# Performance work log

Hardware: AMD Instinct MI355X
Metric: run time of the kernel (lower is better)

## Reference

```python
import jax, jax.numpy as jnp
import numpy as np

IMG_FEAT = 2048
HIDDEN = 1024
K_TIMES = 3
GLIMPSE = 8
BA_HIDDEN = K_TIMES * HIDDEN  # 3072


def setup_inputs() -> dict:
    key = jax.random.key(0)
    ks = jax.random.split(key, 9)
    b, n_v, n_q = 64, 128, 32
    v = jax.random.normal(ks[0], (b, n_v, IMG_FEAT), dtype=jnp.float32)
    q = jax.random.normal(ks[1], (b, n_q, HIDDEN), dtype=jnp.float32)
    # weight-normed Linear params (weight_norm with dim=None -> scalar g)
    v_w = jax.random.normal(ks[2], (BA_HIDDEN, IMG_FEAT), dtype=jnp.float32) * 0.02
    v_g = jnp.asarray(jnp.linalg.norm(v_w), dtype=jnp.float32)
    v_b = jnp.zeros((BA_HIDDEN,), dtype=jnp.float32)
    q_w = jax.random.normal(ks[3], (BA_HIDDEN, HIDDEN), dtype=jnp.float32) * 0.02
    q_g = jnp.asarray(jnp.linalg.norm(q_w), dtype=jnp.float32)
    q_b = jnp.zeros((BA_HIDDEN,), dtype=jnp.float32)
    h_mat = jax.random.normal(ks[4], (1, GLIMPSE, 1, BA_HIDDEN), dtype=jnp.float32)
    h_bias = jax.random.normal(ks[5], (1, GLIMPSE, 1, 1), dtype=jnp.float32)
    return {"v": v, "q": q, "v_w": v_w, "v_g": v_g, "v_b": v_b,
            "q_w": q_w, "q_g": q_g, "q_b": q_b,
            "h_mat": h_mat, "h_bias": h_bias}


def _wn_linear_relu(x, w, g, b):
    # weight_norm(dim=None): w_eff = g * w / ||w||_F (scalar g)
    w_eff = (g / jnp.linalg.norm(w)) * w
    return jax.nn.relu(jnp.einsum('bnd,kd->bnk', x, w_eff) + b)


def reference(v, q, v_w, v_g, v_b, q_w, q_g, q_b, h_mat, h_bias):
    # dropout layers are identity in eval mode
    v_ = _wn_linear_relu(v, v_w, v_g, v_b)  # [b, n_v, K]
    q_ = _wn_linear_relu(q, q_w, q_g, q_b)  # [b, n_q, K]
    # einsum('xhyk,bvk,bqk->bhvq') with h_mat [1,g,1,K]
    hm = h_mat[0, :, 0, :]  # [g, K]
    logits = jnp.einsum('hk,bvk,bqk->bhvq', hm, v_, q_) + h_bias
    return logits
```

## Files before the change

kernel.cpp:

```cpp
#include <hip/hip_runtime.h>

typedef __attribute__((ext_vector_type(8))) __bf16 bf16x8;
typedef __attribute__((ext_vector_type(4))) float f32x4;
typedef const __attribute__((address_space(1))) unsigned int gas_u32;
typedef __attribute__((address_space(3))) unsigned int las_u32;

__device__ __forceinline__ unsigned short f2bf(float f) {
  unsigned u = __builtin_bit_cast(unsigned, f);
  u = (u + 0x7FFFu + ((u >> 16) & 1u)) >> 16;
  return (unsigned short)u;
}
__device__ __forceinline__ float bf2f(unsigned short h) {
  return __builtin_bit_cast(float, (unsigned)h << 16);
}

__global__ __launch_bounds__(256) void k_prep(
    const float* __restrict__ v, const float* __restrict__ q,
    const float* __restrict__ vw, const float* __restrict__ qw,
    unsigned short* __restrict__ v_bf, unsigned short* __restrict__ q_bf,
    unsigned short* __restrict__ vw_bf, unsigned short* __restrict__ qw_bf,
    float* __restrict__ ss) {
  __shared__ float red[4];
  int bid = blockIdx.x, tid = threadIdx.x;
  const float* in;
  unsigned short* out;
  float* ssout = nullptr;
  int n8, b0, nb;
  if (bid < 896) {
    in = v; out = v_bf; n8 = 2097152; b0 = bid; nb = 896;
  } else if (bid < 1008) {
    in = q; out = q_bf; n8 = 262144; b0 = bid - 896; nb = 112;
  } else if (bid < 1360) {
    in = vw; out = vw_bf; n8 = 786432; b0 = bid - 1008; nb = 352; ssout = ss + 0;
  } else {
    in = qw; out = qw_bf; n8 = 393216; b0 = bid - 1360; nb = 176; ssout = ss + 1;
  }
  float s = 0.f;
  for (int i = b0 * 256 + tid; i < n8; i += nb * 256) {
    float4 a = ((const float4*)in)[2 * i];
    float4 b = ((const float4*)in)[2 * i + 1];
    if (ssout) {
      s += a.x * a.x + a.y * a.y + a.z * a.z + a.w * a.w;
      s += b.x * b.x + b.y * b.y + b.z * b.z + b.w * b.w;
    }
    uint4 o;
    o.x = f2bf(a.x) | ((unsigned)f2bf(a.y) << 16);
    o.y = f2bf(a.z) | ((unsigned)f2bf(a.w) << 16);
    o.z = f2bf(b.x) | ((unsigned)f2bf(b.y) << 16);
    o.w = f2bf(b.z) | ((unsigned)f2bf(b.w) << 16);
    ((uint4*)out)[i] = o;
  }
  if (ssout) {
    for (int off = 32; off; off >>= 1) s += __shfl_down(s, off);
    if ((tid & 63) == 0) red[tid >> 6] = s;
    __syncthreads();
    if (tid == 0) atomicAdd(ssout, red[0] + red[1] + red[2] + red[3]);
  }
}

__global__ __launch_bounds__(256, 2) void k_gemm_cmb(
    const unsigned short* __restrict__ A1, const unsigned short* __restrict__ B1,
    const float* __restrict__ bias1, const float* __restrict__ g1,
    const float* __restrict__ ss1, unsigned short* __restrict__ C1,
    const unsigned short* __restrict__ A2, const unsigned short* __restrict__ B2,
    const float* __restrict__ bias2, const float* __restrict__ g2,
    const float* __restrict__ ss2, unsigned short* __restrict__ C2) {
  __shared__ __align__(16) unsigned short lA[2 * 128 * 64];
  __shared__ __align__(16) unsigned short lB[2 * 192 * 64];
  const int tid = threadIdx.x;
  const int wid = tid >> 6, lane = tid & 63;
  const int l15 = lane & 15, l4 = lane >> 4;
  const int wm = wid >> 1, wn = wid & 1;
  const int rr8 = tid >> 3;
  const int scol8 = ((tid & 7) ^ (rr8 & 7)) << 3;

  const unsigned short* A;
  const unsigned short* B;
  const float* bias;
  const float* gptr;
  const float* ssptr;
  unsigned short* C;
  int K, nt, bm, bn;
  if (blockIdx.x < 1024) {
    const int x = blockIdx.x & 7;
    const int idx = blockIdx.x >> 3;
    const int bmHalf = idx >> 6;
    const int rem = idx & 63;
    const int bn_l = rem >> 4;
    const int bm_l = bmHalf * 16 + (rem & 15);
    bm = (x >> 2) * 32 + bm_l;
    bn = (x & 3) * 4 + bn_l;
    A = A1; B = B1; bias = bias1; gptr = g1; ssptr = ss1; C = C1;
    K = 2048; nt = 32;
  } else {
    const int bid = blockIdx.x - 1024;
    const int x = blockIdx.x & 7;
    const int idx = bid >> 3;
    const int bm_l = idx & 7, bn_l = idx >> 3;
    bm = (x >> 2) * 8 + bm_l;
    bn = (x & 3) * 4 + bn_l;
    A = A2; B = B2; bias = bias2; gptr = g2; ssptr = ss2; C = C2;
    K = 1024; nt = 16;
  }

  const unsigned short* Ab = A + (size_t)bm * 128 * K;
  const unsigned short* Bb = B + (size_t)bn * 192 * K;

  const unsigned short* sA00 = Ab + (size_t)(rr8) * K + scol8;
  const unsigned short* sA01 = Ab + (size_t)(32 + rr8) * K + scol8;
  const unsigned short* sA10 = Ab + (size_t)(64 + rr8) * K + scol8;
  const unsigned short* sA11 = Ab + (size_t)(96 + rr8) * K + scol8;
  const unsigned short* sB00 = Bb + (size_t)(rr8) * K + scol8;
  const unsigned short* sB01 = Bb + (size_t)(32 + rr8) * K + scol8;
  const unsigned short* sB10 = Bb + (size_t)(64 + rr8) * K + scol8;
  const unsigned short* sB11 = Bb + (size_t)(96 + rr8) * K + scol8;
  const unsigned short* sB20 = Bb + (size_t)(128 + rr8) * K + scol8;
  const unsigned short* sB21 = Bb + (size_t)(160 + rr8) * K + scol8;

#define SB() __builtin_amdgcn_sched_barrier(0);

#define STAGE_A(U, TS, BUFI)                                                       \
  {                                                                                \
    int ts_ = (TS) < nt ? (TS) : nt - 1;                                           \
    __builtin_amdgcn_global_load_lds(                                              \
        (gas_u32*)(sA##U##0 + (size_t)ts_ * 64),                                   \
        (las_u32*)(lA + (BUFI)*8192 + (U)*4096 + tid * 8), 16, 0, 0);              \
    __builtin_amdgcn_global_load_lds(                                              \
        (gas_u32*)(sA##U##1 + (size_t)ts_ * 64),                                   \
        (las_u32*)(lA + (BUFI)*8192 + (U)*4096 + 2048 + tid * 8), 16, 0, 0);       \
  }

#define STAGE_B(U, TS, BUFI)                                                       \
  {                                                                                \
    int ts_ = (TS) < nt ? (TS) : nt - 1;                                           \
    __builtin_amdgcn_global_load_lds(                                              \
        (gas_u32*)(sB##U##0 + (size_t)ts_ * 64),                                   \
        (las_u32*)(lB + (BUFI)*12288 + (U)*4096 + tid * 8), 16, 0, 0);             \
    __builtin_amdgcn_global_load_lds(                                              \
        (gas_u32*)(sB##U##1 + (size_t)ts_ * 64),                                   \
        (las_u32*)(lB + (BUFI)*12288 + (U)*4096 + 2048 + tid * 8), 16, 0, 0);      \
  }

#define LDSA(DST, MQ, TP)                                                          \
  _Pragma("unroll") for (int i2 = 0; i2 < 2; ++i2) {                               \
    int rl = wm * 64 + ((MQ)*2 + i2) * 16 + l15;                                   \
    const unsigned short* ap = lA + (TP)*8192 + rl * 64;                           \
    int s8 = rl & 7;                                                               \
    DST[i2][0] = *(const bf16x8*)(ap + ((l4 ^ s8) << 3));                          \
    DST[i2][1] = *(const bf16x8*)(ap + (((4 | l4) ^ s8) << 3));                    \
  }

#define LDSB(DST, NQ, TP)                                                          \
  _Pragma("unroll") for (int j3 = 0; j3 < 3; ++j3) {                               \
    int rl = wn * 96 + ((NQ)*3 + j3) * 16 + l15;                                   \
    const unsigned short* bp = lB + (TP)*12288 + rl * 64;                          \
    int s8 = rl & 7;                                                               \
    DST[j3][0] = *(const bf16x8*)(bp + ((l4 ^ s8) << 3));                          \
    DST[j3][1] = *(const bf16x8*)(bp + (((4 | l4) ^ s8) << 3));                    \
  }

#define MFMA12(MQ, NQ, AF, BF)                                                     \
  _Pragma("unroll") for (int ks = 0; ks < 2; ++ks)                                 \
  _Pragma("unroll") for (int i2 = 0; i2 < 2; ++i2)                                 \
  _Pragma("unroll") for (int j3 = 0; j3 < 3; ++j3)                                 \
    acc[(MQ)*2 + i2][(NQ)*3 + j3] = __builtin_amdgcn_mfma_f32_16x16x32_bf16(       \
        AF[i2][ks], BF[j3][ks], acc[(MQ)*2 + i2][(NQ)*3 + j3], 0, 0, 0);

#define TILE_BODY(T, CP, NP)                                                       \
  LDSB(b1_, 1, CP)                                                                 \
  STAGE_B(2, (T) + 1, NP)                                                          \
  __builtin_amdgcn_s_setprio(1);                                                   \
  MFMA12(0, 0, a0_, b0_)                                                           \
  __builtin_amdgcn_s_setprio(0);                                                   \
  LDSA(a1_, 1, CP)                                                                 \
  __builtin_amdgcn_s_setprio(1);                                                   \
  MFMA12(0, 1, a0_, b1_)                                                           \
  __builtin_amdgcn_s_setprio(0);                                                   \
  asm volatile("s_waitcnt lgkmcnt(0)" ::: "memory");                               \
  asm volatile("s_waitcnt vmcnt(6)" ::: "memory");                                 \
  SB()                                                                             \
  __builtin_amdgcn_s_barrier();                                                    \
  LDSA(a0_, 0, NP)                                                                 \
  STAGE_A(0, (T) + 2, CP) STAGE_A(1, (T) + 2, CP)                                  \
  __builtin_amdgcn_s_setprio(1);                                                   \
  MFMA12(1, 0, a1_, b0_)                                                           \
  __builtin_amdgcn_s_setprio(0);                                                   \
  asm volatile("s_waitcnt vmcnt(4)" ::: "memory");                                 \
  SB()                                                                             \
  __builtin_amdgcn_s_barrier();                                                    \
  LDSB(b0_, 0, NP)                                                                 \
  STAGE_B(0, (T) + 2, CP) STAGE_B(1, (T) + 2, CP)                                  \
  __builtin_amdgcn_s_setprio(1);                                                   \
  MFMA12(1, 1, a1_, b1_)                                                           \
  __builtin_amdgcn_s_setprio(0);

  f32x4 acc[4][6] = {};
  bf16x8 a0_[2][2], a1_[2][2], b0_[3][2], b1_[3][2];

  STAGE_A(0, 0, 0) STAGE_A(1, 0, 0) STAGE_B(0, 0, 0) STAGE_B(1, 0, 0) STAGE_B(2, 0, 0)
  STAGE_A(0, 1, 1) STAGE_A(1, 1, 1)
  asm volatile("s_waitcnt vmcnt(4)" ::: "memory");
  SB()
  __builtin_amdgcn_s_barrier();
  LDSA(a0_, 0, 0)
  STAGE_B(0, 1, 1) STAGE_B(1, 1, 1)
  LDSB(b0_, 0, 0)

  for (int t = 0; t < nt; t += 2) {
    TILE_BODY(t, 0, 1)
    TILE_BODY(t + 1, 1, 0)
  }

  asm volatile("s_waitcnt vmcnt(0)" ::: "memory");

  const int N = 3072;
  float s = gptr[0] / sqrtf(ssptr[0]);
#pragma unroll
  for (int nj = 0; nj < 6; ++nj) {
    int gcol = bn * 192 + wn * 96 + nj * 16 + l15;
    float bv = bias[gcol];
#pragma unroll
    for (int mi = 0; mi < 4; ++mi) {
#pragma unroll
      for (int r = 0; r < 4; ++r) {
        int grow = bm * 128 + wm * 64 + mi * 16 + l4 * 4 + r;
        float v = fmaxf(acc[mi][nj][r] * s + bv, 0.f);
        C[(size_t)grow * N + gcol] = f2bf(v);
      }
    }
  }
#undef STAGE_A
#undef STAGE_B
#undef LDSA
#undef LDSB
#undef MFMA12
#undef TILE_BODY
#undef SB
}

__global__ __launch_bounds__(256, 2) void k_glimpse5(
    const unsigned short* __restrict__ Vh, const unsigned short* __restrict__ Qh,
    const float* __restrict__ hmat, const float* __restrict__ hbias,
    float* __restrict__ out) {
  __shared__ __align__(16) unsigned short lV[3][64 * 64];
  __shared__ __align__(16) unsigned short lQ[2][4][32 * 64];
  int tid = threadIdx.x;
  int wid = tid >> 6, lane = tid & 63;
  int l15 = lane & 15, l4 = lane >> 4;

  int id = blockIdx.x;
  int b = id >> 2, hv = id & 3;
  int h4 = hv & 1, vh = hv >> 1;

  const unsigned short* Vb = Vh + (size_t)b * 128 * 3072 + (size_t)vh * 64 * 3072;
  const unsigned short* Qb = Qh + (size_t)b * 32 * 3072;
  const float* hr0 = hmat + (h4 * 4 + 0) * 3072;
  const float* hr1 = hmat + (h4 * 4 + 1) * 3072;
  const float* hr2 = hmat + (h4 * 4 + 2) * 3072;
  const float* hr3 = hmat + (h4 * 4 + 3) * 3072;

  f32x4 acc[4][2] = {};
  const int rr8 = tid >> 3;
  const int ch8 = tid & 7;
  const int scol8 = (ch8 ^ (rr8 & 7)) << 3;
  const int qwoff = rr8 * 64 + scol8;
  const int qc = ch8 * 8;
  const int NT = 48;

#define VSTAGE(T, SLOT)                                                          \
  {                                                                              \
    int tc = (T) < NT ? (T) : NT - 1;                                            \
    _Pragma("unroll") for (int j = 0; j < 2; ++j) {                              \
      __builtin_amdgcn_global_load_lds(                                          \
          (gas_u32*)(Vb + (size_t)(j * 32 + rr8) * 3072 + tc * 64 + scol8),      \
          (las_u32*)(&lV[SLOT][0] + j * 2048 + tid * 8), 16, 0, 0);              \
    }                                                                            \
  }

#define QLOAD(T, RQ, H)                                                          \
  {                                                                              \
    int tc = (T) < NT ? (T) : NT - 1;                                            \
    RQ = *(const uint4*)(Qb + (size_t)rr8 * 3072 + tc * 64 + qc);                \
    H[0] = ((const float4*)(hr0 + tc * 64 + qc))[0];                             \
    H[1] = ((const float4*)(hr0 + tc * 64 + qc))[1];                             \
    H[2] = ((const float4*)(hr1 + tc * 64 + qc))[0];                             \
    H[3] = ((const float4*)(hr1 + tc * 64 + qc))[1];                             \
    H[4] = ((const float4*)(hr2 + tc * 64 + qc))[0];                             \
    H[5] = ((const float4*)(hr2 + tc * 64 + qc))[1];                             \
    H[6] = ((const float4*)(hr3 + tc * 64 + qc))[0];                             \
    H[7] = ((const float4*)(hr3 + tc * 64 + qc))[1];                             \
  }

#define QWRITE(CB, RQ, H)                                                        \
  {                                                                              \
    float e0 = bf2f((unsigned short)(RQ.x & 0xffff));                            \
    float e1 = bf2f((unsigned short)(RQ.x >> 16));                               \
    float e2 = bf2f((unsigned short)(RQ.y & 0xffff));                            \
    float e3 = bf2f((unsigned short)(RQ.y >> 16));                               \
    float e4 = bf2f((unsigned short)(RQ.z & 0xffff));                            \
    float e5 = bf2f((unsigned short)(RQ.z >> 16));                               \
    float e6 = bf2f((unsigned short)(RQ.w & 0xffff));                            \
    float e7 = bf2f((unsigned short)(RQ.w >> 16));                               \
    _Pragma("unroll") for (int hh = 0; hh < 4; ++hh) {                           \
      uint4 o;                                                                   \
      o.x = f2bf(e0 * H[hh * 2].x) | ((unsigned)f2bf(e1 * H[hh * 2].y) << 16);   \
      o.y = f2bf(e2 * H[hh * 2].z) | ((unsigned)f2bf(e3 * H[hh * 2].w) << 16);   \
      o.z = f2bf(e4 * H[hh * 2 + 1].x) |                                         \
            ((unsigned)f2bf(e5 * H[hh * 2 + 1].y) << 16);                        \
      o.w = f2bf(e6 * H[hh * 2 + 1].z) |                                         \
            ((unsigned)f2bf(e7 * H[hh * 2 + 1].w) << 16);                        \
      *(uint4*)(&lQ[CB][hh][0] + qwoff) = o;                                     \
    }                                                                            \
  }

#define GMFMA(SLOT, CB)                                                          \
  {                                                                              \
    int rlv = wid * 16 + l15;                                                    \
    int s8v = rlv & 7;                                                           \
    bf16x8 af[2];                                                                \
    af[0] = *(const bf16x8*)(&lV[SLOT][0] + rlv * 64 + ((l4 ^ s8v) << 3));       \
    af[1] = *(const bf16x8*)(&lV[SLOT][0] + rlv * 64 + (((4 | l4) ^ s8v) << 3)); \
    _Pragma("unroll") for (int hh = 0; hh < 4; ++hh) {                           \
      _Pragma("unroll") for (int nj = 0; nj < 2; ++nj) {                         \
        int rlq = nj * 16 + l15;                                                 \
        int s8q = rlq & 7;                                                       \
        bf16x8 bq0 = *(const bf16x8*)(&lQ[CB][hh][0] + rlq * 64 +                \
                                      ((l4 ^ s8q) << 3));                        \
        bf16x8 bq1 = *(const bf16x8*)(&lQ[CB][hh][0] + rlq * 64 +                \
                                      (((4 | l4) ^ s8q) << 3));                  \
        acc[hh][nj] =                                                            \
            __builtin_amdgcn_mfma_f32_16x16x32_bf16(af[0], bq0, acc[hh][nj], 0, 0, 0); \
        acc[hh][nj] =                                                            \
            __builtin_amdgcn_mfma_f32_16x16x32_bf16(af[1], bq1, acc[hh][nj], 0, 0, 0); \
      }                                                                          \
    }                                                                            \
  }

#define GBODY(T, CQ, CH, NQ, NH)                                                 \
  {                                                                              \
    QLOAD((T) + 2, NQ, NH)                                                       \
    asm volatile("s_waitcnt vmcnt(11)" ::: "memory");                            \
    asm volatile("s_waitcnt lgkmcnt(0)" ::: "memory");                           \
    __builtin_amdgcn_sched_barrier(0);                                           \
    __builtin_amdgcn_s_barrier();                                                \
    VSTAGE((T) + 2, ((T) + 2) % 3)                                               \
    QWRITE(((T) + 1) & 1, CQ, CH)                                                \
    GMFMA((T) % 3, (T) & 1)                                                      \
  }

  uint4 aq, bq_;
  float4 ah[8], bh[8];

  QLOAD(0, aq, ah)
  QLOAD(1, bq_, bh)
  VSTAGE(0, 0)
  VSTAGE(1, 1)
  asm volatile("s_waitcnt vmcnt(13)" ::: "memory");
  __builtin_amdgcn_sched_barrier(0);
  QWRITE(0, aq, ah)

  for (int t = 0; t < NT; t += 2) {
    GBODY(t, bq_, bh, aq, ah)
    GBODY(t + 1, aq, ah, bq_, bh)
  }
  asm volatile("s_waitcnt vmcnt(0) lgkmcnt(0)" ::: "memory");

#pragma unroll
  for (int hh = 0; hh < 4; ++hh) {
    int h = h4 * 4 + hh;
    float hb = hbias[h];
    float* ob = out + (size_t)(b * 8 + h) * 128 * 32;
#pragma unroll
    for (int nj = 0; nj < 2; ++nj)
#pragma unroll
      for (int r = 0; r < 4; ++r) {
        int row = vh * 64 + wid * 16 + l4 * 4 + r;
        int col = nj * 16 + l15;
        ob[row * 32 + col] = acc[hh][nj][r] + hb;
      }
  }
#undef VSTAGE
#undef QLOAD
#undef QWRITE
#undef GMFMA
#undef GBODY
}

extern "C" void kernel_launch(void* const* d_in, const int* in_sizes, int n_in,
                              void* d_out, int out_size, void* d_ws, size_t ws_size,
                              hipStream_t stream) {
  const float* v = (const float*)d_in[0];
  const float* q = (const float*)d_in[1];
  const float* v_w = (const float*)d_in[2];
  const float* v_g = (const float*)d_in[3];
  const float* v_b = (const float*)d_in[4];
  const float* q_w = (const float*)d_in[5];
  const float* q_g = (const float*)d_in[6];
  const float* q_b = (const float*)d_in[7];
  const float* hmat = (const float*)d_in[8];
  const float* hbias = (const float*)d_in[9];
  float* out = (float*)d_out;

  const size_t n_v = 16777216;
  const size_t n_vw = 6291456;
  const size_t n_q = 2097152;
  const size_t n_qw = 3145728;
  const size_t n_vh = 25165824;
  const size_t n_qh = 6291456;

  char* ws = (char*)d_ws;
  float* ss = (float*)ws;
  size_t off = 256;
  unsigned short* v_bf = (unsigned short*)(ws + off);  off += n_v * 2;
  unsigned short* vw_bf = (unsigned short*)(ws + off); off += n_vw * 2;
  unsigned short* q_bf = (unsigned short*)(ws + off);  off += n_q * 2;
  unsigned short* qw_bf = (unsigned short*)(ws + off); off += n_qw * 2;
  unsigned short* v_h = (unsigned short*)(ws + off);   off += n_vh * 2;
  unsigned short* q_h = (unsigned short*)(ws + off);   off += n_qh * 2;

  (void)hipMemsetAsync(ss, 0, 8, stream);
  k_prep<<<1536, 256, 0, stream>>>(v, q, v_w, q_w, v_bf, q_bf, vw_bf, qw_bf, ss);

  k_gemm_cmb<<<1280, 256, 0, stream>>>(v_bf, vw_bf, v_b, v_g, ss + 0, v_h,
                                       q_bf, qw_bf, q_b, q_g, ss + 1, q_h);

  k_glimpse5<<<256, 256, 0, stream>>>(v_h, q_h, hmat, hbias, out);
}
```

Before: 207.3 us.

## Use 256x256 GEMM tiles with 512-thread blocks and XCD-aware tile mapping

The combined V/Q projection GEMM moves from 128x192 tiles on 256-thread blocks to 256x256 tiles on 512-thread blocks with 8 waves. This raises arithmetic intensity per tile and cuts the grid from 1280 to 480 blocks. Tile indices are remapped so consecutive tiles land on the same XCD. The price is one block per CU, larger register and LDS footprints, and coarser load balance across the 256 CUs (480 blocks of unequal K length).

```diff
diff --git a/kernel.cpp b/kernel.cpp
--- a/kernel.cpp
+++ b/kernel.cpp
@@ -58,22 +58,23 @@
   }
 }
 
-__global__ __launch_bounds__(256, 2) void k_gemm_cmb(
+__global__ __launch_bounds__(512, 1) void k_gemm256(
     const unsigned short* __restrict__ A1, const unsigned short* __restrict__ B1,
     const float* __restrict__ bias1, const float* __restrict__ g1,
     const float* __restrict__ ss1, unsigned short* __restrict__ C1,
     const unsigned short* __restrict__ A2, const unsigned short* __restrict__ B2,
     const float* __restrict__ bias2, const float* __restrict__ g2,
     const float* __restrict__ ss2, unsigned short* __restrict__ C2) {
-  __shared__ __align__(16) unsigned short lA[2 * 128 * 64];
-  __shared__ __align__(16) unsigned short lB[2 * 192 * 64];
+  __shared__ __align__(16) unsigned short lA[2 * 4 * 4096];
+  __shared__ __align__(16) unsigned short lB[2 * 4 * 4096];
   const int tid = threadIdx.x;
   const int wid = tid >> 6, lane = tid & 63;
   const int l15 = lane & 15, l4 = lane >> 4;
-  const int wm = wid >> 1, wn = wid & 1;
+  const int wm = wid >> 2, wn = wid & 3;
   const int rr8 = tid >> 3;
   const int scol8 = ((tid & 7) ^ (rr8 & 7)) << 3;
 
+  int wg = (blockIdx.x & 7) * 60 + (blockIdx.x >> 3);
   const unsigned short* A;
   const unsigned short* B;
   const float* bias;
@@ -81,129 +82,104 @@
   const float* ssptr;
   unsigned short* C;
   int K, nt, bm, bn;
-  if (blockIdx.x < 1024) {
-    const int x = blockIdx.x & 7;
-    const int idx = blockIdx.x >> 3;
-    const int bmHalf = idx >> 6;
-    const int rem = idx & 63;
-    const int bn_l = rem >> 4;
-    const int bm_l = bmHalf * 16 + (rem & 15);
-    bm = (x >> 2) * 32 + bm_l;
-    bn = (x & 3) * 4 + bn_l;
+  if (wg < 384) {
+    bm = wg / 12; bn = wg % 12;
     A = A1; B = B1; bias = bias1; gptr = g1; ssptr = ss1; C = C1;
     K = 2048; nt = 32;
   } else {
-    const int bid = blockIdx.x - 1024;
-    const int x = blockIdx.x & 7;
-    const int idx = bid >> 3;
-    const int bm_l = idx & 7, bn_l = idx >> 3;
-    bm = (x >> 2) * 8 + bm_l;
-    bn = (x & 3) * 4 + bn_l;
+    int w2 = wg - 384;
+    bm = w2 / 12; bn = w2 % 12;
     A = A2; B = B2; bias = bias2; gptr = g2; ssptr = ss2; C = C2;
     K = 1024; nt = 16;
   }
 
-  const unsigned short* Ab = A + (size_t)bm * 128 * K;
-  const unsigned short* Bb = B + (size_t)bn * 192 * K;
-
-  const unsigned short* sA00 = Ab + (size_t)(rr8) * K + scol8;
-  const unsigned short* sA01 = Ab + (size_t)(32 + rr8) * K + scol8;
-  const unsigned short* sA10 = Ab + (size_t)(64 + rr8) * K + scol8;
-  const unsigned short* sA11 = Ab + (size_t)(96 + rr8) * K + scol8;
-  const unsigned short* sB00 = Bb + (size_t)(rr8) * K + scol8;
-  const unsigned short* sB01 = Bb + (size_t)(32 + rr8) * K + scol8;
-  const unsigned short* sB10 = Bb + (size_t)(64 + rr8) * K + scol8;
-  const unsigned short* sB11 = Bb + (size_t)(96 + rr8) * K + scol8;
-  const unsigned short* sB20 = Bb + (size_t)(128 + rr8) * K + scol8;
-  const unsigned short* sB21 = Bb + (size_t)(160 + rr8) * K + scol8;
+  const unsigned short* Ab = A + (size_t)bm * 256 * K;
+  const unsigned short* Bb = B + (size_t)bn * 256 * K;
+  const int voffA = rr8 * K + scol8;
+  const int voffB = rr8 * K + scol8;
 
 #define SB() __builtin_amdgcn_sched_barrier(0);
 
-#define STAGE_A(U, TS, BUFI)                                                       \
+#define STAGE_AU(U, TS, BUFI)                                                      \
   {                                                                                \
     int ts_ = (TS) < nt ? (TS) : nt - 1;                                           \
     __builtin_amdgcn_global_load_lds(                                              \
-        (gas_u32*)(sA##U##0 + (size_t)ts_ * 64),                                   \
-        (las_u32*)(lA + (BUFI)*8192 + (U)*4096 + tid * 8), 16, 0, 0);              \
-    __builtin_amdgcn_global_load_lds(                                              \
-        (gas_u32*)(sA##U##1 + (size_t)ts_ * 64),                                   \
-        (las_u32*)(lA + (BUFI)*8192 + (U)*4096 + 2048 + tid * 8), 16, 0, 0);       \
-  }
-
-#define STAGE_B(U, TS, BUFI)                                                       \
+        (gas_u32*)(Ab + (size_t)((U)*64) * K + ts_ * 64 + voffA),                  \
+        (las_u32*)(lA + (BUFI)*16384 + (U)*4096 + tid * 8), 16, 0, 0);             \
+  }
+#define STAGE_BU(U, TS, BUFI)                                                      \
   {                                                                                \
     int ts_ = (TS) < nt ? (TS) : nt - 1;                                           \
     __builtin_amdgcn_global_load_lds(                                              \
-        (gas_u32*)(sB##U##0 + (size_t)ts_ * 64),                                   \
-        (las_u32*)(lB + (BUFI)*12288 + (U)*4096 + tid * 8), 16, 0, 0);             \
-    __builtin_amdgcn_global_load_lds(                                              \
-        (gas_u32*)(sB##U##1 + (size_t)ts_ * 64),                                   \
-        (las_u32*)(lB + (BUFI)*12288 + (U)*4096 + 2048 + tid * 8), 16, 0, 0);      \
-  }
-
-#define LDSA(DST, MQ, TP)                                                          \
-  _Pragma("unroll") for (int i2 = 0; i2 < 2; ++i2) {                               \
-    int rl = wm * 64 + ((MQ)*2 + i2) * 16 + l15;                                   \
-    const unsigned short* ap = lA + (TP)*8192 + rl * 64;                           \
-    int s8 = rl & 7;                                                               \
-    DST[i2][0] = *(const bf16x8*)(ap + ((l4 ^ s8) << 3));                          \
-    DST[i2][1] = *(const bf16x8*)(ap + (((4 | l4) ^ s8) << 3));                    \
-  }
-
-#define LDSB(DST, NQ, TP)                                                          \
-  _Pragma("unroll") for (int j3 = 0; j3 < 3; ++j3) {                               \
-    int rl = wn * 96 + ((NQ)*3 + j3) * 16 + l15;                                   \
-    const unsigned short* bp = lB + (TP)*12288 + rl * 64;                          \
-    int s8 = rl & 7;                                                               \
-    DST[j3][0] = *(const bf16x8*)(bp + ((l4 ^ s8) << 3));                          \
-    DST[j3][1] = *(const bf16x8*)(bp + (((4 | l4) ^ s8) << 3));                    \
-  }
-
-#define MFMA12(MQ, NQ, AF, BF)                                                     \
+        (gas_u32*)(Bb + (size_t)((U)*64) * K + ts_ * 64 + voffB),                  \
+        (las_u32*)(lB + (BUFI)*16384 + (U)*4096 + tid * 8), 16, 0, 0);             \
+  }
+
+#define LDSA(DST, MQ, BUFI)                                                        \
+  _Pragma("unroll") for (int mi = 0; mi < 4; ++mi) {                               \
+    const unsigned short* ap =                                                     \
+        lA + (BUFI)*16384 + (wm * 2 + (MQ)) * 4096 + (mi * 16 + l15) * 64;         \
+    int s8 = l15 & 7;                                                              \
+    DST[mi][0] = *(const bf16x8*)(ap + ((l4 ^ s8) << 3));                          \
+    DST[mi][1] = *(const bf16x8*)(ap + (((4 | l4) ^ s8) << 3));                    \
+  }
+
+#define LDSB(DST, NQ, BUFI)                                                        \
+  _Pragma("unroll") for (int nj = 0; nj < 2; ++nj) {                               \
+    const unsigned short* bp =                                                     \
+        lB + (BUFI)*16384 + wn * 4096 + ((NQ)*32 + nj * 16 + l15) * 64;            \
+    int s8 = l15 & 7;                                                              \
+    DST[nj][0] = *(const bf16x8*)(bp + ((l4 ^ s8) << 3));                          \
+    DST[nj][1] = *(const bf16x8*)(bp + (((4 | l4) ^ s8) << 3));                    \
+  }
+
+#define MFMAQ(MQ, NQ, AF, BF)                                                      \
   _Pragma("unroll") for (int ks = 0; ks < 2; ++ks)                                 \
-  _Pragma("unroll") for (int i2 = 0; i2 < 2; ++i2)                                 \
-  _Pragma("unroll") for (int j3 = 0; j3 < 3; ++j3)                                 \
-    acc[(MQ)*2 + i2][(NQ)*3 + j3] = __builtin_amdgcn_mfma_f32_16x16x32_bf16(       \
-        AF[i2][ks], BF[j3][ks], acc[(MQ)*2 + i2][(NQ)*3 + j3], 0, 0, 0);
+  _Pragma("unroll") for (int mi = 0; mi < 4; ++mi)                                 \
+  _Pragma("unroll") for (int nj = 0; nj < 2; ++nj)                                 \
+    acc[(MQ)*4 + mi][(NQ)*2 + nj] = __builtin_amdgcn_mfma_f32_16x16x32_bf16(       \
+        AF[mi][ks], BF[nj][ks], acc[(MQ)*4 + mi][(NQ)*2 + nj], 0, 0, 0);
 
 #define TILE_BODY(T, CP, NP)                                                       \
   LDSB(b1_, 1, CP)                                                                 \
-  STAGE_B(2, (T) + 1, NP)                                                          \
+  STAGE_BU(2, (T) + 1, NP) STAGE_BU(3, (T) + 1, NP)                                \
   __builtin_amdgcn_s_setprio(1);                                                   \
-  MFMA12(0, 0, a0_, b0_)                                                           \
+  MFMAQ(0, 0, a0_, b0_)                                                            \
   __builtin_amdgcn_s_setprio(0);                                                   \
   LDSA(a1_, 1, CP)                                                                 \
   __builtin_amdgcn_s_setprio(1);                                                   \
-  MFMA12(0, 1, a0_, b1_)                                                           \
+  MFMAQ(0, 1, a0_, b1_)                                                            \
   __builtin_amdgcn_s_setprio(0);                                                   \
   asm volatile("s_waitcnt lgkmcnt(0)" ::: "memory");                               \
-  asm volatile("s_waitcnt vmcnt(6)" ::: "memory");                                 \
+  asm volatile("s_waitcnt vmcnt(4)" ::: "memory");                                 \
   SB()                                                                             \
   __builtin_amdgcn_s_barrier();                                                    \
   LDSA(a0_, 0, NP)                                                                 \
-  STAGE_A(0, (T) + 2, CP) STAGE_A(1, (T) + 2, CP)                                  \
+  STAGE_AU(0, (T) + 2, CP) STAGE_AU(1, (T) + 2, CP)                                \
+  STAGE_AU(2, (T) + 2, CP) STAGE_AU(3, (T) + 2, CP)                                \
   __builtin_amdgcn_s_setprio(1);                                                   \
-  MFMA12(1, 0, a1_, b0_)                                                           \
+  MFMAQ(1, 0, a1_, b0_)                                                            \
   __builtin_amdgcn_s_setprio(0);                                                   \
   asm volatile("s_waitcnt vmcnt(4)" ::: "memory");                                 \
   SB()                                                                             \
   __builtin_amdgcn_s_barrier();                                                    \
   LDSB(b0_, 0, NP)                                                                 \
-  STAGE_B(0, (T) + 2, CP) STAGE_B(1, (T) + 2, CP)                                  \
+  STAGE_BU(0, (T) + 2, CP) STAGE_BU(1, (T) + 2, CP)                                \
   __builtin_amdgcn_s_setprio(1);                                                   \
-  MFMA12(1, 1, a1_, b1_)                                                           \
+  MFMAQ(1, 1, a1_, b1_)                                                            \
   __builtin_amdgcn_s_setprio(0);
 
-  f32x4 acc[4][6] = {};
-  bf16x8 a0_[2][2], a1_[2][2], b0_[3][2], b1_[3][2];
-
-  STAGE_A(0, 0, 0) STAGE_A(1, 0, 0) STAGE_B(0, 0, 0) STAGE_B(1, 0, 0) STAGE_B(2, 0, 0)
-  STAGE_A(0, 1, 1) STAGE_A(1, 1, 1)
-  asm volatile("s_waitcnt vmcnt(4)" ::: "memory");
+  f32x4 acc[8][4] = {};
+  bf16x8 a0_[4][2], a1_[4][2], b0_[2][2], b1_[2][2];
+
+  STAGE_AU(0, 0, 0) STAGE_AU(1, 0, 0) STAGE_AU(2, 0, 0) STAGE_AU(3, 0, 0)
+  STAGE_BU(0, 0, 0) STAGE_BU(1, 0, 0) STAGE_BU(2, 0, 0) STAGE_BU(3, 0, 0)
+  STAGE_AU(0, 1, 1) STAGE_AU(1, 1, 1) STAGE_AU(2, 1, 1) STAGE_AU(3, 1, 1)
+  STAGE_BU(0, 1, 1) STAGE_BU(1, 1, 1)
+  asm volatile("s_waitcnt vmcnt(6)" ::: "memory");
   SB()
   __builtin_amdgcn_s_barrier();
   LDSA(a0_, 0, 0)
-  STAGE_B(0, 1, 1) STAGE_B(1, 1, 1)
   LDSB(b0_, 0, 0)
 
   for (int t = 0; t < nt; t += 2) {
@@ -216,24 +192,27 @@
   const int N = 3072;
   float s = gptr[0] / sqrtf(ssptr[0]);
 #pragma unroll
-  for (int nj = 0; nj < 6; ++nj) {
-    int gcol = bn * 192 + wn * 96 + nj * 16 + l15;
-    float bv = bias[gcol];
-#pragma unroll
-    for (int mi = 0; mi < 4; ++mi) {
-#pragma unroll
-      for (int r = 0; r < 4; ++r) {
-        int grow = bm * 128 + wm * 64 + mi * 16 + l4 * 4 + r;
-        float v = fmaxf(acc[mi][nj][r] * s + bv, 0.f);
-        C[(size_t)grow * N + gcol] = f2bf(v);
-      }
+  for (int nq = 0; nq < 2; ++nq)
+#pragma unroll
+    for (int nj = 0; nj < 2; ++nj) {
+      int gcol = bn * 256 + wn * 64 + nq * 32 + nj * 16 + l15;
+      float bv = bias[gcol];
+#pragma unroll
+      for (int mq = 0; mq < 2; ++mq)
+#pragma unroll
+        for (int mi = 0; mi < 4; ++mi)
+#pragma unroll
+          for (int r = 0; r < 4; ++r) {
+            int grow = bm * 256 + wm * 128 + mq * 64 + mi * 16 + l4 * 4 + r;
+            float v = fmaxf(acc[mq * 4 + mi][nq * 2 + nj][r] * s + bv, 0.f);
+            C[(size_t)grow * N + gcol] = f2bf(v);
+          }
     }
-  }
-#undef STAGE_A
-#undef STAGE_B
+#undef STAGE_AU
+#undef STAGE_BU
 #undef LDSA
 #undef LDSB
-#undef MFMA12
+#undef MFMAQ
 #undef TILE_BODY
 #undef SB
 }
@@ -421,8 +400,8 @@
   (void)hipMemsetAsync(ss, 0, 8, stream);
   k_prep<<<1536, 256, 0, stream>>>(v, q, v_w, q_w, v_bf, q_bf, vw_bf, qw_bf, ss);
 
-  k_gemm_cmb<<<1280, 256, 0, stream>>>(v_bf, vw_bf, v_b, v_g, ss + 0, v_h,
-                                       q_bf, qw_bf, q_b, q_g, ss + 1, q_h);
+  k_gemm256<<<480, 512, 0, stream>>>(v_bf, vw_bf, v_b, v_g, ss + 0, v_h,
+                                     q_bf, qw_bf, q_b, q_g, ss + 1, q_h);
 
   k_glimpse5<<<256, 256, 0, stream>>>(v_h, q_h, hmat, hbias, out);
 }
```

After: 221.3 us. 6.7% more time.
